# Kernel tuning notes

Measured on AMD Instinct MI355X. Metric: run time of the kernel, lower is better.

## Reference

```python
import jax, jax.numpy as jnp
import numpy as np

P = 1024          # nodes per graph
B = 64            # graphs in batch
N = P * B         # total nodes
E = N * 32        # total edges (avg degree 32)
D_IN = 16         # per-node feature dim (share_obs_dim)
H = 32            # GCN / MLP hidden dim (hardcoded in GNet)
SHARE = 64        # flat share_state dim


def setup_inputs() -> dict:
    key = jax.random.key(0)
    ks = jax.random.split(key, 20)

    x = jax.random.normal(ks[0], (N, D_IN), jnp.float32)
    src = jax.random.randint(ks[1], (E,), 0, N, dtype=jnp.int32)
    # keep edges inside each 1024-node graph block (PyG batched graphs)
    dst = (src // P) * P + jax.random.randint(ks[2], (E,), 0, P, dtype=jnp.int32)
    edge_index = jnp.stack([src, dst])
    value_batch = (jnp.arange(N, dtype=jnp.int32) // P)
    share_state = jax.random.normal(ks[3], (B, SHARE), jnp.float32)

    def lin(k, o, i):
        return jax.random.normal(k, (o, i), jnp.float32) / np.float32(np.sqrt(i))

    return {
        "x": x, "edge_index": edge_index, "value_batch": value_batch,
        "share_state": share_state,
        # value_gnet: GCNConv(D_IN,32), GCNConv(32,32), Linear(32,32), post-pool Linear(32,32)
        "W1": lin(ks[4], H, D_IN), "b1": jnp.zeros((H,), jnp.float32),
        "W2": lin(ks[5], H, H),    "b2": jnp.zeros((H,), jnp.float32),
        "Wl": lin(ks[6], H, H),    "bl": jnp.zeros((H,), jnp.float32),
        "Wp": lin(ks[7], H, H),    "bp": jnp.zeros((H,), jnp.float32),
        # value_net MLP: SHARE->32->32->32
        "Vw1": lin(ks[8], H, SHARE), "Vb1": jnp.zeros((H,), jnp.float32),
        "Vw2": lin(ks[9], H, H),     "Vb2": jnp.zeros((H,), jnp.float32),
        "Vw3": lin(ks[10], H, H),    "Vb3": jnp.zeros((H,), jnp.float32),
        # value_comnet: 64->32->1
        "Cw1": lin(ks[11], H, 2 * H), "Cb1": jnp.zeros((H,), jnp.float32),
        "Cw2": lin(ks[12], 1, H) * np.float32(0.01), "Cb2": jnp.zeros((1,), jnp.float32),
    }


def gcn_conv(x, src, dst, W, b):
    """PyG GCNConv: D^-1/2 (A+I) D^-1/2 X W^T + b (unit edge weights)."""
    n = x.shape[0]
    loop = jnp.arange(n, dtype=src.dtype)
    s = jnp.concatenate([src, loop])
    d = jnp.concatenate([dst, loop])
    deg = jax.ops.segment_sum(jnp.ones(s.shape[0], x.dtype), d, num_segments=n)
    dis = jnp.where(deg > 0, jax.lax.rsqrt(jnp.maximum(deg, 1e-12)), 0.0)
    norm = dis[s] * dis[d]                      # [E+N]
    h = x @ W.T                                  # [N, H] small GEMM first
    out = jax.ops.segment_sum(h[s] * norm[:, None], d, num_segments=n)
    return out + b


def reference(x, edge_index, value_batch, share_state,
              W1, b1, W2, b2, Wl, bl, Wp, bp,
              Vw1, Vb1, Vw2, Vb2, Vw3, Vb3,
              Cw1, Cb1, Cw2, Cb2):
    src, dst = edge_index[0], edge_index[1]
    nb = share_state.shape[0]

    # value_gnet
    h = jnp.tanh(gcn_conv(x, src, dst, W1, b1))
    h = jnp.tanh(gcn_conv(h, src, dst, W2, b2))
    h = jnp.tanh(h @ Wl.T + bl)
    pooled = jax.ops.segment_sum(h, value_batch, num_segments=nb)  # global_add_pool -> [B, 32]
    h1 = pooled @ Wp.T + bp

    # value_net MLP on flat share_state
    h2 = jnp.tanh(share_state @ Vw1.T + Vb1)
    h2 = jnp.tanh(h2 @ Vw2.T + Vb2)
    h2 = h2 @ Vw3.T + Vb3

    # value_comnet
    z = jnp.tanh(jnp.concatenate([h1, h2], axis=-1) @ Cw1.T + Cb1)
    value = z @ Cw2.T + Cb2                      # [B, 1]
    return value
```

## Files before the change

### kernel.cpp

```cpp
#include <hip/hip_runtime.h>
#include <math.h>

#define NNODES 65536
#define NEDGES 2097152
#define PGRAPH 1024
#define NGRAPH 64
#define CAPB   9216
#define CAPQ   9728

#define OFF_GFILL 0u
#define OFF_ARR   1024u
#define OFF_POOL4 1536u
#define OFF_DIS   34304u
#define OFF_EBUF  296448u
#define OFF_H1G   9733632u

__device__ __forceinline__ float ftanh(float x) {
    float e = __expf(2.f * x);
    return 1.f - 2.f * __builtin_amdgcn_rcpf(e + 1.f);
}

__global__ void k_bucket(const int* __restrict__ src, const int* __restrict__ dst,
                         int* __restrict__ gfill, unsigned int* __restrict__ ebuf) {
    __shared__ unsigned int sorted[8192];
    __shared__ int hist[256], lexcl[256], gbase[256], lfill[256];
    __shared__ int wsum[4];
    int t = threadIdx.x;
    hist[t] = 0; lfill[t] = 0;
    __syncthreads();

    const int4* src4 = (const int4*)(src + blockIdx.x * 8192);
    const int4* dst4 = (const int4*)(dst + blockIdx.x * 8192);
    unsigned int pk[32];
    #pragma unroll
    for (int k = 0; k < 8; k++) {
        int4 s4 = src4[k * 256 + t];
        int4 d4 = dst4[k * 256 + t];
        int ss[4] = { s4.x, s4.y, s4.z, s4.w };
        int dd[4] = { d4.x, d4.y, d4.z, d4.w };
        #pragma unroll
        for (int j = 0; j < 4; j++) {
            int g = ss[j] >> 10;
            pk[k * 4 + j] = (unsigned int)((ss[j] & 1023) | ((dd[j] & 1023) << 10) | (g << 20));
            int b = (g << 2) | ((dd[j] >> 8) & 3);
            atomicAdd(&hist[b], 1);
        }
    }
    __syncthreads();

    int h = hist[t];
    int lane = t & 63, wid = t >> 6;
    int xx = h;
    #pragma unroll
    for (int off = 1; off < 64; off <<= 1) {
        int y = __shfl_up(xx, off, 64);
        if (lane >= off) xx += y;
    }
    if (lane == 63) wsum[wid] = xx;
    __syncthreads();
    {
        int pre = 0;
        for (int w = 0; w < wid; w++) pre += wsum[w];
        lexcl[t] = pre + xx - h;
        gbase[t] = atomicAdd(&gfill[t], h);
    }
    __syncthreads();

    #pragma unroll
    for (int k = 0; k < 32; k++) {
        int b = pk[k] >> 18;
        int pos = lexcl[b] + atomicAdd(&lfill[b], 1);
        sorted[pos] = pk[k];
    }
    __syncthreads();
    for (int i = t; i < 8192; i += 256) {
        unsigned int p = sorted[i];
        int b = p >> 18;
        ebuf[(size_t)b * CAPB + gbase[b] + (i - lexcl[b])] = p;
    }
}

__global__ __launch_bounds__(1024, 1) void k_gcn(
        const float* __restrict__ x,
        const float* __restrict__ W1, const float* __restrict__ b1,
        const float* __restrict__ W2, const float* __restrict__ b2,
        const float* __restrict__ Wl, const float* __restrict__ bl,
        const unsigned int* __restrict__ ebuf, const int* __restrict__ gfill,
        float* __restrict__ disg, float* __restrict__ h1g,
        int* __restrict__ arrive, float* __restrict__ pooled4) {
    __shared__ float hsL[1025 * 32];
    __shared__ unsigned short lcsr[CAPQ];
    __shared__ float WlL[32 * 33];
    __shared__ int hist[256], lrow[256], lfill[256];
    __shared__ int wsum[4];
    float4* hsL4 = (float4*)hsL;

    int t = threadIdx.x;
    int g = blockIdx.x & 63, part = blockIdx.x >> 6;
    int bkt = (g << 2) | part;
    int cnt = gfill[bkt];
    const unsigned int* eb = ebuf + (size_t)bkt * CAPB;

    float inr[16];
    {
        const float4* in4 = (const float4*)(x + ((size_t)(g << 10) + t) * 16);
        #pragma unroll
        for (int k = 0; k < 4; k++) {
            float4 v = in4[k];
            inr[4*k] = v.x; inr[4*k+1] = v.y; inr[4*k+2] = v.z; inr[4*k+3] = v.w;
        }
    }

    if (t < 256) hist[t] = 0;
    WlL[(t >> 5) * 33 + (t & 31)] = Wl[t];
    if (t < 32) hsL[1024 * 32 + t] = 0.f;
    __syncthreads();

    for (int i = t; i < cnt; i += 1024) atomicAdd(&hist[(eb[i] >> 10) & 255], 1);
    __syncthreads();

    int dq = 0, r4 = 0;
    if (t < 256) {
        dq = hist[t]; r4 = (dq + 3) & ~3;
        disg[(g << 10) + part * 256 + t] = rsqrtf((float)(dq + 1));
    }
    __syncthreads();
    if (t == 0)
        __hip_atomic_fetch_add(arrive + g, 1, __ATOMIC_RELEASE, __HIP_MEMORY_SCOPE_AGENT);

    int lane = t & 63, wid = t >> 6;
    int xx = r4;
    #pragma unroll
    for (int off = 1; off < 64; off <<= 1) {
        int y = __shfl_up(xx, off, 64);
        if (lane >= off) xx += y;
    }
    if (t < 256 && lane == 63) wsum[wid] = xx;
    __syncthreads();
    if (t < 256) {
        int pre = 0;
        for (int w = 0; w < wid; w++) pre += wsum[w];
        lrow[t] = pre + xx - r4;
        lfill[t] = 0;
    }
    __syncthreads();

    for (int i = t; i < cnt; i += 1024) {
        unsigned int v = eb[i];
        int dl = (v >> 10) & 255;
        int pos = lrow[dl] + atomicAdd(&lfill[dl], 1);
        lcsr[pos] = (unsigned short)(v & 1023);
    }
    if (t < 256) {
        int st = lrow[t];
        for (int i = dq; i < r4; i++) lcsr[st + i] = 1024;
    }

    if (t == 0) {
        while (__hip_atomic_load(arrive + g, __ATOMIC_RELAXED, __HIP_MEMORY_SCOPE_AGENT) < 4) {}
        (void)__hip_atomic_load(arrive + g, __ATOMIC_ACQUIRE, __HIP_MEMORY_SCOPE_AGENT);
    }
    __syncthreads();

    float dis_t = disg[(g << 10) + t];
    int sw = t & 7;

    #pragma unroll
    for (int o4 = 0; o4 < 8; o4++) {
        float r[4];
        #pragma unroll
        for (int j = 0; j < 4; j++) {
            int o = o4 * 4 + j;
            float s = 0.f;
            #pragma unroll
            for (int k = 0; k < 16; k++) s += inr[k] * W1[o * 16 + k];
            r[j] = s * dis_t;
        }
        hsL4[t * 8 + (o4 ^ sw)] = make_float4(r[0], r[1], r[2], r[3]);
    }
    __syncthreads();

    int q = t & 7, grp = t >> 3;
    #pragma unroll
    for (int pass = 0; pass < 2; pass++) {
        int lq = pass * 128 + grp;
        int ln = part * 256 + lq;
        int d = hist[lq];
        float dn = rsqrtf((float)(d + 1));
        int st = lrow[lq];
        float4 acc = hsL4[ln * 8 + (q ^ (ln & 7))];
        const ushort4* c4 = (const ushort4*)(lcsr + st);
        int d4 = (d + 3) >> 2;
        for (int i = 0; i < d4; i++) {
            ushort4 ss = c4[i];
            float4 v0 = hsL4[ss.x * 8 + (q ^ (ss.x & 7))];
            float4 v1 = hsL4[ss.y * 8 + (q ^ (ss.y & 7))];
            float4 v2 = hsL4[ss.z * 8 + (q ^ (ss.z & 7))];
            float4 v3 = hsL4[ss.w * 8 + (q ^ (ss.w & 7))];
            acc.x += (v0.x + v1.x) + (v2.x + v3.x);
            acc.y += (v0.y + v1.y) + (v2.y + v3.y);
            acc.z += (v0.z + v1.z) + (v2.z + v3.z);
            acc.w += (v0.w + v1.w) + (v2.w + v3.w);
        }
        float4 bb = ((const float4*)b1)[q];
        float4 r;
        r.x = ftanh(dn * acc.x + bb.x);
        r.y = ftanh(dn * acc.y + bb.y);
        r.z = ftanh(dn * acc.z + bb.z);
        r.w = ftanh(dn * acc.w + bb.w);
        ((float4*)h1g)[((size_t)(g << 10) + ln) * 8 + q] = r;
    }
    __syncthreads();
    if (t == 0) {
        __hip_atomic_fetch_add(arrive + 64 + g, 1, __ATOMIC_RELEASE, __HIP_MEMORY_SCOPE_AGENT);
        while (__hip_atomic_load(arrive + 64 + g, __ATOMIC_RELAXED, __HIP_MEMORY_SCOPE_AGENT) < 4) {}
        (void)__hip_atomic_load(arrive + 64 + g, __ATOMIC_ACQUIRE, __HIP_MEMORY_SCOPE_AGENT);
    }
    __syncthreads();

    float r2[32];
    {
        const float4* h4 = (const float4*)(h1g + ((size_t)(g << 10) + t) * 32);
        #pragma unroll
        for (int k = 0; k < 8; k++) {
            float4 v = h4[k];
            r2[4*k] = v.x; r2[4*k+1] = v.y; r2[4*k+2] = v.z; r2[4*k+3] = v.w;
        }
    }
    #pragma unroll
    for (int o4 = 0; o4 < 8; o4++) {
        float r[4];
        #pragma unroll
        for (int j = 0; j < 4; j++) {
            int o = o4 * 4 + j;
            float s = 0.f;
            #pragma unroll
            for (int k = 0; k < 32; k++) s += r2[k] * W2[o * 32 + k];
            r[j] = s * dis_t;
        }
        hsL4[t * 8 + (o4 ^ sw)] = make_float4(r[0], r[1], r[2], r[3]);
    }
    __syncthreads();

    float4 racc[2];
    #pragma unroll
    for (int pass = 0; pass < 2; pass++) {
        int lq = pass * 128 + grp;
        int ln = part * 256 + lq;
        int d = hist[lq];
        float dn = rsqrtf((float)(d + 1));
        int st = lrow[lq];
        float4 acc = hsL4[ln * 8 + (q ^ (ln & 7))];
        const ushort4* c4 = (const ushort4*)(lcsr + st);
        int d4 = (d + 3) >> 2;
        for (int i = 0; i < d4; i++) {
            ushort4 ss = c4[i];
            float4 v0 = hsL4[ss.x * 8 + (q ^ (ss.x & 7))];
            float4 v1 = hsL4[ss.y * 8 + (q ^ (ss.y & 7))];
            float4 v2 = hsL4[ss.z * 8 + (q ^ (ss.z & 7))];
            float4 v3 = hsL4[ss.w * 8 + (q ^ (ss.w & 7))];
            acc.x += (v0.x + v1.x) + (v2.x + v3.x);
            acc.y += (v0.y + v1.y) + (v2.y + v3.y);
            acc.z += (v0.z + v1.z) + (v2.z + v3.z);
            acc.w += (v0.w + v1.w) + (v2.w + v3.w);
        }
        float4 bb = ((const float4*)b2)[q];
        float4 r;
        r.x = ftanh(dn * acc.x + bb.x);
        r.y = ftanh(dn * acc.y + bb.y);
        r.z = ftanh(dn * acc.z + bb.z);
        r.w = ftanh(dn * acc.w + bb.w);
        racc[pass] = r;
    }

    __syncthreads();
    #pragma unroll
    for (int pass = 0; pass < 2; pass++) {
        int lnn = pass * 128 + grp;
        hsL4[lnn * 8 + (q ^ (lnn & 7))] = racc[pass];
    }
    __syncthreads();
    int o = t & 31, seg = t >> 5;
    float ps = 0.f;
    #pragma unroll
    for (int j = 0; j < 8; j++) {
        int nl = seg * 8 + j;
        int swn = nl & 7;
        float s = bl[o];
        #pragma unroll
        for (int k = 0; k < 32; k++) {
            float h2v = hsL[nl * 32 + ((((k >> 2) ^ swn) << 2) | (k & 3))];
            s += h2v * WlL[o * 33 + k];
        }
        ps += ftanh(s);
    }
    float* psum = hsL + 8192;
    psum[t] = ps;
    __syncthreads();
    if (t < 32) {
        float tot = 0.f;
        for (int s = 0; s < 32; s++) tot += psum[s * 32 + t];
        pooled4[(g * 4 + part) * 32 + t] = tot;
    }
}

__global__ void k_final(const float* __restrict__ pooled4, const float* __restrict__ share,
                        const float* __restrict__ Wp,  const float* __restrict__ bp,
                        const float* __restrict__ Vw1, const float* __restrict__ Vb1,
                        const float* __restrict__ Vw2, const float* __restrict__ Vb2,
                        const float* __restrict__ Vw3, const float* __restrict__ Vb3,
                        const float* __restrict__ Cw1, const float* __restrict__ Cb1,
                        const float* __restrict__ Cw2, const float* __restrict__ Cb2,
                        float* __restrict__ out) {
    int id = blockIdx.x * 256 + threadIdx.x;
    int b = id >> 5;
    int j = id & 31;
    float p = pooled4[(b * 4 + 0) * 32 + j] + pooled4[(b * 4 + 1) * 32 + j]
            + pooled4[(b * 4 + 2) * 32 + j] + pooled4[(b * 4 + 3) * 32 + j];
    float h1v = bp[j];
    #pragma unroll
    for (int k = 0; k < 32; k++) h1v += Wp[j * 32 + k] * __shfl(p, k, 32);
    float s0 = share[b * 64 + j];
    float s1 = share[b * 64 + 32 + j];
    float t1 = Vb1[j];
    #pragma unroll
    for (int k = 0; k < 32; k++) {
        t1 += Vw1[j * 64 + k] * __shfl(s0, k, 32);
        t1 += Vw1[j * 64 + 32 + k] * __shfl(s1, k, 32);
    }
    t1 = tanhf(t1);
    float t2 = Vb2[j];
    #pragma unroll
    for (int k = 0; k < 32; k++) t2 += Vw2[j * 32 + k] * __shfl(t1, k, 32);
    t2 = tanhf(t2);
    float h2v = Vb3[j];
    #pragma unroll
    for (int k = 0; k < 32; k++) h2v += Vw3[j * 32 + k] * __shfl(t2, k, 32);
    float z = Cb1[j];
    #pragma unroll
    for (int k = 0; k < 32; k++) {
        z += Cw1[j * 64 + k] * __shfl(h1v, k, 32);
        z += Cw1[j * 64 + 32 + k] * __shfl(h2v, k, 32);
    }
    z = tanhf(z);
    float v = Cw2[j] * z;
    v += __shfl_down(v, 16, 32); v += __shfl_down(v, 8, 32);
    v += __shfl_down(v, 4, 32);  v += __shfl_down(v, 2, 32);
    v += __shfl_down(v, 1, 32);
    if (j == 0) out[b] = v + Cb2[0];
}

extern "C" void kernel_launch(void* const* d_in, const int* in_sizes, int n_in,
                              void* d_out, int out_size, void* d_ws, size_t ws_size,
                              hipStream_t stream) {
    const float* x     = (const float*)d_in[0];
    const int*   ei    = (const int*)d_in[1];
    const float* share = (const float*)d_in[3];
    const float* W1 = (const float*)d_in[4];  const float* b1 = (const float*)d_in[5];
    const float* W2 = (const float*)d_in[6];  const float* b2 = (const float*)d_in[7];
    const float* Wl = (const float*)d_in[8];  const float* bl = (const float*)d_in[9];
    const float* Wp = (const float*)d_in[10]; const float* bp = (const float*)d_in[11];
    const float* Vw1 = (const float*)d_in[12]; const float* Vb1 = (const float*)d_in[13];
    const float* Vw2 = (const float*)d_in[14]; const float* Vb2 = (const float*)d_in[15];
    const float* Vw3 = (const float*)d_in[16]; const float* Vb3 = (const float*)d_in[17];
    const float* Cw1 = (const float*)d_in[18]; const float* Cb1 = (const float*)d_in[19];
    const float* Cw2 = (const float*)d_in[20]; const float* Cb2 = (const float*)d_in[21];

    char* ws = (char*)d_ws;
    int*          gfill   = (int*)(ws + OFF_GFILL);
    int*          arrive  = (int*)(ws + OFF_ARR);
    float*        pooled4 = (float*)(ws + OFF_POOL4);
    float*        disg    = (float*)(ws + OFF_DIS);
    unsigned int* ebuf    = (unsigned int*)(ws + OFF_EBUF);
    float*        h1g     = (float*)(ws + OFF_H1G);

    const int* srcp = ei;
    const int* dstp = ei + NEDGES;

    hipMemsetAsync(ws, 0, 1536, stream);

    k_bucket<<<256, 256, 0, stream>>>(srcp, dstp, gfill, ebuf);
    k_gcn<<<256, 1024, 0, stream>>>(x, W1, b1, W2, b2, Wl, bl,
                                    ebuf, gfill, disg, h1g, arrive, pooled4);
    k_final<<<8, 256, 0, stream>>>(pooled4, share, Wp, bp, Vw1, Vb1, Vw2, Vb2,
                                   Vw3, Vb3, Cw1, Cb1, Cw2, Cb2, (float*)d_out);
}
```

Baseline: 179.2 us.

## Fuse bucketing, GCN and final MLP into one persistent kernel with grid barriers

Merges the edge-bucketing kernel, the GCN kernel and the final MLP kernel into a single 256-block launch. Blocks first bucket their edge slice, then wait on a global atomic counter before the GCN phase. A per-graph arrival counter lets part 0 of each graph compute the output head. This removes two kernel launches and their inter-kernel gaps, at the cost of spin-wait grid barriers that assume all 256 blocks are co-resident. It also reads the Wl weights into registers instead of staging them in shared memory.

```diff
diff --git a/kernel.cpp b/kernel.cpp
--- a/kernel.cpp
+++ b/kernel.cpp
@@ -1,118 +1,137 @@
 #include <hip/hip_runtime.h>
 #include <math.h>
 
-#define NNODES 65536
 #define NEDGES 2097152
-#define PGRAPH 1024
-#define NGRAPH 64
 #define CAPB   9216
 #define CAPQ   9728
 
 #define OFF_GFILL 0u
-#define OFF_ARR   1024u
-#define OFF_POOL4 1536u
-#define OFF_DIS   34304u
-#define OFF_EBUF  296448u
-#define OFF_H1G   9733632u
+#define OFF_CTR   1024u
+#define OFF_ARR1  1152u
+#define OFF_ARR2  1408u
+#define OFF_ARR3  1664u
+#define OFF_POOL4 2048u
+#define OFF_DIS   34816u
+#define OFF_H1G   296960u
+#define OFF_EBUF  8685568u
 
 __device__ __forceinline__ float ftanh(float x) {
     float e = __expf(2.f * x);
     return 1.f - 2.f * __builtin_amdgcn_rcpf(e + 1.f);
 }
 
-__global__ void k_bucket(const int* __restrict__ src, const int* __restrict__ dst,
-                         int* __restrict__ gfill, unsigned int* __restrict__ ebuf) {
-    __shared__ unsigned int sorted[8192];
-    __shared__ int hist[256], lexcl[256], gbase[256], lfill[256];
-    __shared__ int wsum[4];
-    int t = threadIdx.x;
-    hist[t] = 0; lfill[t] = 0;
-    __syncthreads();
-
-    const int4* src4 = (const int4*)(src + blockIdx.x * 8192);
-    const int4* dst4 = (const int4*)(dst + blockIdx.x * 8192);
-    unsigned int pk[32];
-    #pragma unroll
-    for (int k = 0; k < 8; k++) {
-        int4 s4 = src4[k * 256 + t];
-        int4 d4 = dst4[k * 256 + t];
-        int ss[4] = { s4.x, s4.y, s4.z, s4.w };
-        int dd[4] = { d4.x, d4.y, d4.z, d4.w };
-        #pragma unroll
-        for (int j = 0; j < 4; j++) {
-            int g = ss[j] >> 10;
-            pk[k * 4 + j] = (unsigned int)((ss[j] & 1023) | ((dd[j] & 1023) << 10) | (g << 20));
-            int b = (g << 2) | ((dd[j] >> 8) & 3);
-            atomicAdd(&hist[b], 1);
-        }
-    }
-    __syncthreads();
-
-    int h = hist[t];
-    int lane = t & 63, wid = t >> 6;
-    int xx = h;
-    #pragma unroll
-    for (int off = 1; off < 64; off <<= 1) {
-        int y = __shfl_up(xx, off, 64);
-        if (lane >= off) xx += y;
-    }
-    if (lane == 63) wsum[wid] = xx;
-    __syncthreads();
-    {
-        int pre = 0;
-        for (int w = 0; w < wid; w++) pre += wsum[w];
-        lexcl[t] = pre + xx - h;
-        gbase[t] = atomicAdd(&gfill[t], h);
-    }
-    __syncthreads();
-
-    #pragma unroll
-    for (int k = 0; k < 32; k++) {
-        int b = pk[k] >> 18;
-        int pos = lexcl[b] + atomicAdd(&lfill[b], 1);
-        sorted[pos] = pk[k];
-    }
-    __syncthreads();
-    for (int i = t; i < 8192; i += 256) {
-        unsigned int p = sorted[i];
-        int b = p >> 18;
-        ebuf[(size_t)b * CAPB + gbase[b] + (i - lexcl[b])] = p;
-    }
-}
-
-__global__ __launch_bounds__(1024, 1) void k_gcn(
+__global__ __launch_bounds__(1024, 1) void k_main(
         const float* __restrict__ x,
+        const int* __restrict__ src, const int* __restrict__ dst,
         const float* __restrict__ W1, const float* __restrict__ b1,
         const float* __restrict__ W2, const float* __restrict__ b2,
         const float* __restrict__ Wl, const float* __restrict__ bl,
-        const unsigned int* __restrict__ ebuf, const int* __restrict__ gfill,
-        float* __restrict__ disg, float* __restrict__ h1g,
-        int* __restrict__ arrive, float* __restrict__ pooled4) {
+        const float* __restrict__ Wp, const float* __restrict__ bp,
+        const float* __restrict__ Vw1, const float* __restrict__ Vb1,
+        const float* __restrict__ Vw2, const float* __restrict__ Vb2,
+        const float* __restrict__ Vw3, const float* __restrict__ Vb3,
+        const float* __restrict__ Cw1, const float* __restrict__ Cb1,
+        const float* __restrict__ Cw2, const float* __restrict__ Cb2,
+        const float* __restrict__ share,
+        int* __restrict__ gfill, int* __restrict__ ctr,
+        int* __restrict__ arr1, int* __restrict__ arr2, int* __restrict__ arr3,
+        unsigned int* __restrict__ ebuf, float* __restrict__ disg,
+        float* __restrict__ h1g, float* __restrict__ pooled4,
+        float* __restrict__ out) {
     __shared__ float hsL[1025 * 32];
     __shared__ unsigned short lcsr[CAPQ];
-    __shared__ float WlL[32 * 33];
-    __shared__ int hist[256], lrow[256], lfill[256];
+    __shared__ int hist[256], lrow[256], lfill[256], gbase[256];
     __shared__ int wsum[4];
     float4* hsL4 = (float4*)hsL;
+    unsigned int* sorted = (unsigned int*)hsL;
 
     int t = threadIdx.x;
-    int g = blockIdx.x & 63, part = blockIdx.x >> 6;
+    int blk = blockIdx.x;
+    int lane = t & 63, wid = t >> 6;
+
+    if (t < 256) { hist[t] = 0; lfill[t] = 0; }
+    __syncthreads();
+
+    unsigned int pk[8];
+    {
+        const int4* s4p = (const int4*)(src + blk * 8192);
+        const int4* d4p = (const int4*)(dst + blk * 8192);
+        #pragma unroll
+        for (int k = 0; k < 2; k++) {
+            int4 s4 = s4p[k * 1024 + t];
+            int4 d4 = d4p[k * 1024 + t];
+            int ss[4] = { s4.x, s4.y, s4.z, s4.w };
+            int dd[4] = { d4.x, d4.y, d4.z, d4.w };
+            #pragma unroll
+            for (int j = 0; j < 4; j++) {
+                int gg = ss[j] >> 10;
+                pk[k * 4 + j] = (unsigned int)((ss[j] & 1023) | ((dd[j] & 1023) << 10) | (gg << 20));
+                atomicAdd(&hist[(gg << 2) | ((dd[j] >> 8) & 3)], 1);
+            }
+        }
+    }
+    __syncthreads();
+
+    int hA = 0, xxA = 0;
+    if (t < 256) {
+        hA = hist[t];
+        xxA = hA;
+        #pragma unroll
+        for (int off = 1; off < 64; off <<= 1) {
+            int y = __shfl_up(xxA, off, 64);
+            if (lane >= off) xxA += y;
+        }
+        if (lane == 63) wsum[wid] = xxA;
+    }
+    __syncthreads();
+    if (t < 256) {
+        int pre = 0;
+        for (int w = 0; w < wid; w++) pre += wsum[w];
+        lrow[t] = pre + xxA - hA;
+        gbase[t] = atomicAdd(&gfill[t], hA);
+    }
+    __syncthreads();
+
+    #pragma unroll
+    for (int k = 0; k < 8; k++) {
+        int b = pk[k] >> 18;
+        int pos = lrow[b] + atomicAdd(&lfill[b], 1);
+        sorted[pos] = pk[k];
+    }
+    __syncthreads();
+    #pragma unroll
+    for (int k = 0; k < 8; k++) {
+        int i = k * 1024 + t;
+        unsigned int p = sorted[i];
+        int b = p >> 18;
+        ebuf[(size_t)b * CAPB + gbase[b] + (i - lrow[b])] = p;
+    }
+    __syncthreads();
+    if (t == 0)
+        __hip_atomic_fetch_add(ctr, 1, __ATOMIC_RELEASE, __HIP_MEMORY_SCOPE_AGENT);
+
+    int g = blk & 63, part = blk >> 6;
+
+    float inr[16];
+    {
+        const float4* in4 = (const float4*)(x + ((size_t)((g << 10) + t)) * 16);
+        #pragma unroll
+        for (int k = 0; k < 4; k++) {
+            float4 v = in4[k];
+            inr[4*k] = v.x; inr[4*k+1] = v.y; inr[4*k+2] = v.z; inr[4*k+3] = v.w;
+        }
+    }
+    if (t == 0) {
+        while (__hip_atomic_load(ctr, __ATOMIC_RELAXED, __HIP_MEMORY_SCOPE_AGENT) < 256) {}
+        (void)__hip_atomic_load(ctr, __ATOMIC_ACQUIRE, __HIP_MEMORY_SCOPE_AGENT);
+    }
+    __syncthreads();
+
     int bkt = (g << 2) | part;
     int cnt = gfill[bkt];
     const unsigned int* eb = ebuf + (size_t)bkt * CAPB;
 
-    float inr[16];
-    {
-        const float4* in4 = (const float4*)(x + ((size_t)(g << 10) + t) * 16);
-        #pragma unroll
-        for (int k = 0; k < 4; k++) {
-            float4 v = in4[k];
-            inr[4*k] = v.x; inr[4*k+1] = v.y; inr[4*k+2] = v.z; inr[4*k+3] = v.w;
-        }
-    }
-
     if (t < 256) hist[t] = 0;
-    WlL[(t >> 5) * 33 + (t & 31)] = Wl[t];
     if (t < 32) hsL[1024 * 32 + t] = 0.f;
     __syncthreads();
 
@@ -126,9 +145,8 @@
     }
     __syncthreads();
     if (t == 0)
-        __hip_atomic_fetch_add(arrive + g, 1, __ATOMIC_RELEASE, __HIP_MEMORY_SCOPE_AGENT);
-
-    int lane = t & 63, wid = t >> 6;
+        __hip_atomic_fetch_add(arr1 + g, 1, __ATOMIC_RELEASE, __HIP_MEMORY_SCOPE_AGENT);
+
     int xx = r4;
     #pragma unroll
     for (int off = 1; off < 64; off <<= 1) {
@@ -157,8 +175,8 @@
     }
 
     if (t == 0) {
-        while (__hip_atomic_load(arrive + g, __ATOMIC_RELAXED, __HIP_MEMORY_SCOPE_AGENT) < 4) {}
-        (void)__hip_atomic_load(arrive + g, __ATOMIC_ACQUIRE, __HIP_MEMORY_SCOPE_AGENT);
+        while (__hip_atomic_load(arr1 + g, __ATOMIC_RELAXED, __HIP_MEMORY_SCOPE_AGENT) < 4) {}
+        (void)__hip_atomic_load(arr1 + g, __ATOMIC_ACQUIRE, __HIP_MEMORY_SCOPE_AGENT);
     }
     __syncthreads();
 
@@ -212,9 +230,9 @@
     }
     __syncthreads();
     if (t == 0) {
-        __hip_atomic_fetch_add(arrive + 64 + g, 1, __ATOMIC_RELEASE, __HIP_MEMORY_SCOPE_AGENT);
-        while (__hip_atomic_load(arrive + 64 + g, __ATOMIC_RELAXED, __HIP_MEMORY_SCOPE_AGENT) < 4) {}
-        (void)__hip_atomic_load(arrive + 64 + g, __ATOMIC_ACQUIRE, __HIP_MEMORY_SCOPE_AGENT);
+        __hip_atomic_fetch_add(arr2 + g, 1, __ATOMIC_RELEASE, __HIP_MEMORY_SCOPE_AGENT);
+        while (__hip_atomic_load(arr2 + g, __ATOMIC_RELAXED, __HIP_MEMORY_SCOPE_AGENT) < 4) {}
+        (void)__hip_atomic_load(arr2 + g, __ATOMIC_ACQUIRE, __HIP_MEMORY_SCOPE_AGENT);
     }
     __syncthreads();
 
@@ -282,72 +300,79 @@
     __syncthreads();
     int o = t & 31, seg = t >> 5;
     float ps = 0.f;
-    #pragma unroll
-    for (int j = 0; j < 8; j++) {
-        int nl = seg * 8 + j;
-        int swn = nl & 7;
-        float s = bl[o];
-        #pragma unroll
-        for (int k = 0; k < 32; k++) {
-            float h2v = hsL[nl * 32 + ((((k >> 2) ^ swn) << 2) | (k & 3))];
-            s += h2v * WlL[o * 33 + k];
-        }
-        ps += ftanh(s);
+    {
+        float wlr[32];
+        #pragma unroll
+        for (int k = 0; k < 32; k++) wlr[k] = Wl[o * 32 + k];
+        float blv = bl[o];
+        #pragma unroll
+        for (int j = 0; j < 8; j++) {
+            int nl = seg * 8 + j;
+            int swn = nl & 7;
+            float s = blv;
+            #pragma unroll
+            for (int k = 0; k < 32; k++) {
+                float h2v = hsL[nl * 32 + ((((k >> 2) ^ swn) << 2) | (k & 3))];
+                s += h2v * wlr[k];
+            }
+            ps += ftanh(s);
+        }
     }
     float* psum = hsL + 8192;
     psum[t] = ps;
     __syncthreads();
     if (t < 32) {
         float tot = 0.f;
-        for (int s = 0; s < 32; s++) tot += psum[s * 32 + t];
+        for (int s2 = 0; s2 < 32; s2++) tot += psum[s2 * 32 + t];
         pooled4[(g * 4 + part) * 32 + t] = tot;
     }
-}
-
-__global__ void k_final(const float* __restrict__ pooled4, const float* __restrict__ share,
-                        const float* __restrict__ Wp,  const float* __restrict__ bp,
-                        const float* __restrict__ Vw1, const float* __restrict__ Vb1,
-                        const float* __restrict__ Vw2, const float* __restrict__ Vb2,
-                        const float* __restrict__ Vw3, const float* __restrict__ Vb3,
-                        const float* __restrict__ Cw1, const float* __restrict__ Cb1,
-                        const float* __restrict__ Cw2, const float* __restrict__ Cb2,
-                        float* __restrict__ out) {
-    int id = blockIdx.x * 256 + threadIdx.x;
-    int b = id >> 5;
-    int j = id & 31;
-    float p = pooled4[(b * 4 + 0) * 32 + j] + pooled4[(b * 4 + 1) * 32 + j]
-            + pooled4[(b * 4 + 2) * 32 + j] + pooled4[(b * 4 + 3) * 32 + j];
-    float h1v = bp[j];
-    #pragma unroll
-    for (int k = 0; k < 32; k++) h1v += Wp[j * 32 + k] * __shfl(p, k, 32);
-    float s0 = share[b * 64 + j];
-    float s1 = share[b * 64 + 32 + j];
-    float t1 = Vb1[j];
-    #pragma unroll
-    for (int k = 0; k < 32; k++) {
-        t1 += Vw1[j * 64 + k] * __shfl(s0, k, 32);
-        t1 += Vw1[j * 64 + 32 + k] * __shfl(s1, k, 32);
-    }
-    t1 = tanhf(t1);
-    float t2 = Vb2[j];
-    #pragma unroll
-    for (int k = 0; k < 32; k++) t2 += Vw2[j * 32 + k] * __shfl(t1, k, 32);
-    t2 = tanhf(t2);
-    float h2v = Vb3[j];
-    #pragma unroll
-    for (int k = 0; k < 32; k++) h2v += Vw3[j * 32 + k] * __shfl(t2, k, 32);
-    float z = Cb1[j];
-    #pragma unroll
-    for (int k = 0; k < 32; k++) {
-        z += Cw1[j * 64 + k] * __shfl(h1v, k, 32);
-        z += Cw1[j * 64 + 32 + k] * __shfl(h2v, k, 32);
-    }
-    z = tanhf(z);
-    float v = Cw2[j] * z;
-    v += __shfl_down(v, 16, 32); v += __shfl_down(v, 8, 32);
-    v += __shfl_down(v, 4, 32);  v += __shfl_down(v, 2, 32);
-    v += __shfl_down(v, 1, 32);
-    if (j == 0) out[b] = v + Cb2[0];
+
+    __syncthreads();
+    if (t == 0)
+        __hip_atomic_fetch_add(arr3 + g, 1, __ATOMIC_RELEASE, __HIP_MEMORY_SCOPE_AGENT);
+    if (part == 0) {
+        if (t == 0) {
+            while (__hip_atomic_load(arr3 + g, __ATOMIC_RELAXED, __HIP_MEMORY_SCOPE_AGENT) < 4) {}
+            (void)__hip_atomic_load(arr3 + g, __ATOMIC_ACQUIRE, __HIP_MEMORY_SCOPE_AGENT);
+        }
+        __syncthreads();
+        if (t < 32) {
+            int j = t;
+            float p = pooled4[(g * 4 + 0) * 32 + j] + pooled4[(g * 4 + 1) * 32 + j]
+                    + pooled4[(g * 4 + 2) * 32 + j] + pooled4[(g * 4 + 3) * 32 + j];
+            float h1v = bp[j];
+            #pragma unroll
+            for (int k = 0; k < 32; k++) h1v += Wp[j * 32 + k] * __shfl(p, k, 32);
+            float s0 = share[g * 64 + j];
+            float s1 = share[g * 64 + 32 + j];
+            float t1 = Vb1[j];
+            #pragma unroll
+            for (int k = 0; k < 32; k++) {
+                t1 += Vw1[j * 64 + k] * __shfl(s0, k, 32);
+                t1 += Vw1[j * 64 + 32 + k] * __shfl(s1, k, 32);
+            }
+            t1 = tanhf(t1);
+            float t2 = Vb2[j];
+            #pragma unroll
+            for (int k = 0; k < 32; k++) t2 += Vw2[j * 32 + k] * __shfl(t1, k, 32);
+            t2 = tanhf(t2);
+            float h2v = Vb3[j];
+            #pragma unroll
+            for (int k = 0; k < 32; k++) h2v += Vw3[j * 32 + k] * __shfl(t2, k, 32);
+            float z = Cb1[j];
+            #pragma unroll
+            for (int k = 0; k < 32; k++) {
+                z += Cw1[j * 64 + k] * __shfl(h1v, k, 32);
+                z += Cw1[j * 64 + 32 + k] * __shfl(h2v, k, 32);
+            }
+            z = tanhf(z);
+            float v = Cw2[j] * z;
+            v += __shfl_down(v, 16, 32); v += __shfl_down(v, 8, 32);
+            v += __shfl_down(v, 4, 32);  v += __shfl_down(v, 2, 32);
+            v += __shfl_down(v, 1, 32);
+            if (j == 0) out[g] = v + Cb2[0];
+        }
+    }
 }
 
 extern "C" void kernel_launch(void* const* d_in, const int* in_sizes, int n_in,
@@ -368,20 +393,24 @@
 
     char* ws = (char*)d_ws;
     int*          gfill   = (int*)(ws + OFF_GFILL);
-    int*          arrive  = (int*)(ws + OFF_ARR);
+    int*          ctr     = (int*)(ws + OFF_CTR);
+    int*          arr1    = (int*)(ws + OFF_ARR1);
+    int*          arr2    = (int*)(ws + OFF_ARR2);
+    int*          arr3    = (int*)(ws + OFF_ARR3);
     float*        pooled4 = (float*)(ws + OFF_POOL4);
     float*        disg    = (float*)(ws + OFF_DIS);
+    float*        h1g     = (float*)(ws + OFF_H1G);
     unsigned int* ebuf    = (unsigned int*)(ws + OFF_EBUF);
-    float*        h1g     = (float*)(ws + OFF_H1G);
 
     const int* srcp = ei;
     const int* dstp = ei + NEDGES;
 
-    hipMemsetAsync(ws, 0, 1536, stream);
-
-    k_bucket<<<256, 256, 0, stream>>>(srcp, dstp, gfill, ebuf);
-    k_gcn<<<256, 1024, 0, stream>>>(x, W1, b1, W2, b2, Wl, bl,
-                                    ebuf, gfill, disg, h1g, arrive, pooled4);
-    k_final<<<8, 256, 0, stream>>>(pooled4, share, Wp, bp, Vw1, Vb1, Vw2, Vb2,
-                                   Vw3, Vb3, Cw1, Cb1, Cw2, Cb2, (float*)d_out);
+    hipMemsetAsync(ws, 0, 2048, stream);
+
+    k_main<<<256, 1024, 0, stream>>>(x, srcp, dstp,
+                                     W1, b1, W2, b2, Wl, bl, Wp, bp,
+                                     Vw1, Vb1, Vw2, Vb2, Vw3, Vb3,
+                                     Cw1, Cb1, Cw2, Cb2, share,
+                                     gfill, ctr, arr1, arr2, arr3,
+                                     ebuf, disg, h1g, pooled4, (float*)d_out);
 }
```

Result: slower. 205.0 us (+14.4%).
